# Optimization experiments

Measured on AMD Instinct MI355X. Metric: run time of the kernel, lower is better.

The kernel has to match this reference:

```python
import jax, jax.numpy as jnp
import numpy as np

EPS = 1e-12  # torch F.normalize eps

def setup_inputs() -> dict:
    key = jax.random.key(0)
    k1, k2 = jax.random.split(key)
    N, M, D = 256, 2000, 128
    gene_seq = jax.random.randint(k1, (N, M), 0, 4)
    embedding_mat = jax.random.normal(k2, (M, 4, D), dtype=jnp.float32) * (np.sqrt(2.0) / D)
    return {"gene_seq": gene_seq, "embedding_mat": embedding_mat}

def reference(gene_seq, embedding_mat):
    # L2-normalize each (gene, base) row along embedding dim (torch F.normalize semantics)
    norm = jnp.linalg.norm(embedding_mat, axis=-1, keepdims=True)
    table = embedding_mat / jnp.maximum(norm, EPS)  # (M, 4, D)
    M = table.shape[0]
    # One-hot einsum 'nmi,nmid->nmd' == direct gather of row gene_seq[n,m] at position m
    gene_idx = jnp.arange(M)[None, :]               # (1, M)
    out = table[gene_idx, gene_seq, :]              # (N, M, D)
    return out
```

## Files before the change

### kernel.cpp

```cpp
#include <hip/hip_runtime.h>


#define N_SEQ   256
#define M_GENES 2000
#define D_DIM   128
#define ROWS    (M_GENES * 4)
#define P2_BX   25
#define P2_IT   10

typedef float vfloat4 __attribute__((ext_vector_type(4)));

__global__ __launch_bounds__(256) void inv_norm_kernel(
    const float* __restrict__ emb,
    float*       __restrict__ inv_norm)
{
    const int idx = blockIdx.x * 256 + threadIdx.x;
    const int row = idx >> 5;
    const int c   = idx & 31;

    const vfloat4 v = *reinterpret_cast<const vfloat4*>(emb + ((row << 7) + (c << 2)));
    float ss = v.x * v.x + v.y * v.y + v.z * v.z + v.w * v.w;
    ss += __shfl_xor(ss, 1, 32);
    ss += __shfl_xor(ss, 2, 32);
    ss += __shfl_xor(ss, 4, 32);
    ss += __shfl_xor(ss, 8, 32);
    ss += __shfl_xor(ss, 16, 32);
    const float inv = 1.0f / fmaxf(sqrtf(ss), 1e-12f);
    if (c == 0) inv_norm[row] = inv;
}

__global__ __launch_bounds__(256) void gather_scale_kernel(
    const int*   __restrict__ gene_seq,
    const float* __restrict__ emb,
    const float* __restrict__ inv_norm,
    float*       __restrict__ out)
{
    const int n = blockIdx.y;
    const int* __restrict__ gs = gene_seq + n * M_GENES;
    float* __restrict__ outn = out + (size_t)n * (M_GENES * D_DIM);

    const int j0 = blockIdx.x * 256 + threadIdx.x;

    #pragma unroll
    for (int it = 0; it < P2_IT; ++it) {
        const int j = j0 + it * (P2_BX * 256);
        const int m = j >> 5;
        const int c = j & 31;

        const int   g   = gs[m];
        const int   row = (m << 2) + g;
        const float inv = inv_norm[row];
        const vfloat4 v = *reinterpret_cast<const vfloat4*>(emb + ((row << 7) + (c << 2)));

        vfloat4 o = v * inv;
        __builtin_nontemporal_store(o, reinterpret_cast<vfloat4*>(outn + ((size_t)j << 2)));
    }
}

extern "C" void kernel_launch(void* const* d_in, const int* in_sizes, int n_in,
                              void* d_out, int out_size, void* d_ws, size_t ws_size,
                              hipStream_t stream) {
    const int*   gene_seq = (const int*)d_in[0];
    const float* emb      = (const float*)d_in[1];
    float*       out      = (float*)d_out;
    float*       inv_norm = (float*)d_ws;

    inv_norm_kernel<<<dim3(ROWS * 32 / 256), dim3(256), 0, stream>>>(emb, inv_norm);

    gather_scale_kernel<<<dim3(P2_BX, N_SEQ), dim3(256), 0, stream>>>(
        gene_seq, emb, inv_norm, out);
}
```

Before: 270.8 us.

## Precompute normalized table and XCD-aware tiled gather over gene tiles

The first kernel now writes a fully normalized copy of the embedding table to the workspace, so the gather kernel only copies rows and skips the per-element inv_norm load and multiply. The gather is reorganized into 64-gene tiles per block, with the block id remapped so that each XCD handles a fixed set of four gene tiles across all sequences. Each XCD's L2 then only has to hold a slice of the table. This adds a 4 MB table write, and the last tile needs a bounds-checked path.

```diff
diff --git a/kernel.cpp b/kernel.cpp
--- a/kernel.cpp
+++ b/kernel.cpp
@@ -1,24 +1,26 @@
 #include <hip/hip_runtime.h>
 
 
-#define N_SEQ   256
-#define M_GENES 2000
-#define D_DIM   128
-#define ROWS    (M_GENES * 4)
-#define P2_BX   25
-#define P2_IT   10
+#define N_SEQ     256
+#define M_GENES   2000
+#define D_DIM     128
+#define ROWS      (M_GENES * 4)
+#define P1_BLOCKS (ROWS * 32 / 256)
+#define TILE_M    64
+#define N_TILES   32
+#define P2_IT     8
+#define P2_BLOCKS (N_TILES * N_SEQ)
 
 typedef float vfloat4 __attribute__((ext_vector_type(4)));
 
-__global__ __launch_bounds__(256) void inv_norm_kernel(
+__global__ __launch_bounds__(256) void norm_table_kernel(
     const float* __restrict__ emb,
-    float*       __restrict__ inv_norm)
+    float*       __restrict__ tableN)
 {
     const int idx = blockIdx.x * 256 + threadIdx.x;
-    const int row = idx >> 5;
-    const int c   = idx & 31;
+    const int off = idx << 2;
 
-    const vfloat4 v = *reinterpret_cast<const vfloat4*>(emb + ((row << 7) + (c << 2)));
+    const vfloat4 v = *reinterpret_cast<const vfloat4*>(emb + off);
     float ss = v.x * v.x + v.y * v.y + v.z * v.z + v.w * v.w;
     ss += __shfl_xor(ss, 1, 32);
     ss += __shfl_xor(ss, 2, 32);
@@ -26,34 +28,48 @@
     ss += __shfl_xor(ss, 8, 32);
     ss += __shfl_xor(ss, 16, 32);
     const float inv = 1.0f / fmaxf(sqrtf(ss), 1e-12f);
-    if (c == 0) inv_norm[row] = inv;
+
+    const vfloat4 o = v * inv;
+    *reinterpret_cast<vfloat4*>(tableN + off) = o;
 }
 
-__global__ __launch_bounds__(256) void gather_scale_kernel(
+__global__ __launch_bounds__(256) void gather_kernel(
     const int*   __restrict__ gene_seq,
-    const float* __restrict__ emb,
-    const float* __restrict__ inv_norm,
+    const float* __restrict__ tableN,
     float*       __restrict__ out)
 {
-    const int n = blockIdx.y;
-    const int* __restrict__ gs = gene_seq + n * M_GENES;
-    float* __restrict__ outn = out + (size_t)n * (M_GENES * D_DIM);
+    const int id   = blockIdx.x;
+    const int xcd  = id & 7;
+    const int q    = id >> 3;
+    const int tile = (xcd << 2) | (q >> 8);
+    const int n    = q & 255;
 
-    const int j0 = blockIdx.x * 256 + threadIdx.x;
+    const int* __restrict__ gs   = gene_seq + n * M_GENES;
+    float*     __restrict__ outn = out + (size_t)n * (M_GENES * D_DIM);
+    const int m0 = tile * TILE_M;
 
-    #pragma unroll
-    for (int it = 0; it < P2_IT; ++it) {
-        const int j = j0 + it * (P2_BX * 256);
-        const int m = j >> 5;
-        const int c = j & 31;
-
-        const int   g   = gs[m];
-        const int   row = (m << 2) + g;
-        const float inv = inv_norm[row];
-        const vfloat4 v = *reinterpret_cast<const vfloat4*>(emb + ((row << 7) + (c << 2)));
-
-        vfloat4 o = v * inv;
-        __builtin_nontemporal_store(o, reinterpret_cast<vfloat4*>(outn + ((size_t)j << 2)));
+    if (m0 + TILE_M <= M_GENES) {
+        #pragma unroll
+        for (int it = 0; it < P2_IT; ++it) {
+            const int u   = it * 256 + threadIdx.x;
+            const int m   = m0 + (u >> 5);
+            const int c4  = (u & 31) << 2;
+            const int row = (m << 2) + gs[m];
+            const vfloat4 v = *reinterpret_cast<const vfloat4*>(tableN + (row << 7) + c4);
+            __builtin_nontemporal_store(v, reinterpret_cast<vfloat4*>(outn + (m << 7) + c4));
+        }
+    } else {
+        #pragma unroll
+        for (int it = 0; it < P2_IT; ++it) {
+            const int u = it * 256 + threadIdx.x;
+            const int m = m0 + (u >> 5);
+            if (m < M_GENES) {
+                const int c4  = (u & 31) << 2;
+                const int row = (m << 2) + gs[m];
+                const vfloat4 v = *reinterpret_cast<const vfloat4*>(tableN + (row << 7) + c4);
+                __builtin_nontemporal_store(v, reinterpret_cast<vfloat4*>(outn + (m << 7) + c4));
+            }
+        }
     }
 }
 
@@ -63,10 +79,9 @@
     const int*   gene_seq = (const int*)d_in[0];
     const float* emb      = (const float*)d_in[1];
     float*       out      = (float*)d_out;
-    float*       inv_norm = (float*)d_ws;
+    float*       tableN   = (float*)d_ws;
 
-    inv_norm_kernel<<<dim3(ROWS * 32 / 256), dim3(256), 0, stream>>>(emb, inv_norm);
+    norm_table_kernel<<<dim3(P1_BLOCKS), dim3(256), 0, stream>>>(emb, tableN);
 
-    gather_scale_kernel<<<dim3(P2_BX, N_SEQ), dim3(256), 0, stream>>>(
-        gene_seq, emb, inv_norm, out);
+    gather_kernel<<<dim3(P2_BLOCKS), dim3(256), 0, stream>>>(gene_seq, tableN, out);
 }
```

Measured after the change: 272.0 us. Within noise of the previous version (+0.4%).

## Fuse normalization into gather with per-gene register-resident normalized rows

Applied to the files above, without the earlier changes.

Replaces the two-kernel pipeline (inverse-norm precompute plus gather-and-scale) with one kernel. Each half-wave loads and normalizes all four base rows for one gene into registers, then loops over 64 sequences, picking the row by the gene_seq value broadcast with shuffles. This removes the second launch, the workspace round-trip and the repeated embedding reads per sequence. In exchange, the normalization is recomputed by each of the four sequence-chunk blocks, gene_seq is read with a strided pattern, and output stores change from nontemporal to regular, with each store spread across 64 sequence rows.

```diff
diff --git a/kernel.cpp b/kernel.cpp
--- a/kernel.cpp
+++ b/kernel.cpp
@@ -4,56 +4,58 @@
 #define N_SEQ   256
 #define M_GENES 2000
 #define D_DIM   128
-#define ROWS    (M_GENES * 4)
-#define P2_BX   25
-#define P2_IT   10
+#define GENES_PER_BLOCK 8
+#define N_CHUNK 64
+#define GRID_X  (M_GENES / GENES_PER_BLOCK)
+#define GRID_Y  (N_SEQ / N_CHUNK)
 
 typedef float vfloat4 __attribute__((ext_vector_type(4)));
 
-__global__ __launch_bounds__(256) void inv_norm_kernel(
-    const float* __restrict__ emb,
-    float*       __restrict__ inv_norm)
-{
-    const int idx = blockIdx.x * 256 + threadIdx.x;
-    const int row = idx >> 5;
-    const int c   = idx & 31;
-
-    const vfloat4 v = *reinterpret_cast<const vfloat4*>(emb + ((row << 7) + (c << 2)));
-    float ss = v.x * v.x + v.y * v.y + v.z * v.z + v.w * v.w;
-    ss += __shfl_xor(ss, 1, 32);
-    ss += __shfl_xor(ss, 2, 32);
-    ss += __shfl_xor(ss, 4, 32);
-    ss += __shfl_xor(ss, 8, 32);
-    ss += __shfl_xor(ss, 16, 32);
-    const float inv = 1.0f / fmaxf(sqrtf(ss), 1e-12f);
-    if (c == 0) inv_norm[row] = inv;
-}
-
-__global__ __launch_bounds__(256) void gather_scale_kernel(
+__global__ __launch_bounds__(256) void fused_gather_kernel(
     const int*   __restrict__ gene_seq,
     const float* __restrict__ emb,
-    const float* __restrict__ inv_norm,
     float*       __restrict__ out)
 {
-    const int n = blockIdx.y;
-    const int* __restrict__ gs = gene_seq + n * M_GENES;
-    float* __restrict__ outn = out + (size_t)n * (M_GENES * D_DIM);
+    const int tid  = threadIdx.x;
+    const int wave = tid >> 6;
+    const int lane = tid & 63;
+    const int c    = lane & 31;
 
-    const int j0 = blockIdx.x * 256 + threadIdx.x;
+    const int m0    = blockIdx.x * GENES_PER_BLOCK;
+    const int n0    = blockIdx.y * N_CHUNK;
+    const int m_sel = m0 + (wave << 1) + (lane >> 5);
 
+    vfloat4 r[4];
     #pragma unroll
-    for (int it = 0; it < P2_IT; ++it) {
-        const int j = j0 + it * (P2_BX * 256);
-        const int m = j >> 5;
-        const int c = j & 31;
+    for (int g = 0; g < 4; ++g) {
+        const vfloat4 v = *reinterpret_cast<const vfloat4*>(
+            emb + (((m_sel << 2) + g) << 7) + (c << 2));
+        float ss = v.x * v.x + v.y * v.y + v.z * v.z + v.w * v.w;
+        ss += __shfl_xor(ss, 1, 32);
+        ss += __shfl_xor(ss, 2, 32);
+        ss += __shfl_xor(ss, 4, 32);
+        ss += __shfl_xor(ss, 8, 32);
+        ss += __shfl_xor(ss, 16, 32);
+        const float inv = 1.0f / fmaxf(sqrtf(ss), 1e-12f);
+        r[g] = v * inv;
+    }
 
-        const int   g   = gs[m];
-        const int   row = (m << 2) + g;
-        const float inv = inv_norm[row];
-        const vfloat4 v = *reinterpret_cast<const vfloat4*>(emb + ((row << 7) + (c << 2)));
+    const int g0 = gene_seq[(n0 + c)      * M_GENES + m_sel];
+    const int g1 = gene_seq[(n0 + 32 + c) * M_GENES + m_sel];
 
-        vfloat4 o = v * inv;
-        __builtin_nontemporal_store(o, reinterpret_cast<vfloat4*>(outn + ((size_t)j << 2)));
+    float* __restrict__ outbase = out + (size_t)(m_sel << 7) + (c << 2);
+
+    #pragma unroll 4
+    for (int n = 0; n < N_CHUNK; ++n) {
+        const int src = (lane & 32) | (n & 31);
+        const int gv  = __shfl((n < 32) ? g0 : g1, src, 64);
+
+        const vfloat4 lo = (gv & 1) ? r[1] : r[0];
+        const vfloat4 hi = (gv & 1) ? r[3] : r[2];
+        const vfloat4 v  = (gv & 2) ? hi : lo;
+
+        *reinterpret_cast<vfloat4*>(
+            outbase + (size_t)(n0 + n) * (M_GENES * D_DIM)) = v;
     }
 }
 
@@ -63,10 +65,7 @@
     const int*   gene_seq = (const int*)d_in[0];
     const float* emb      = (const float*)d_in[1];
     float*       out      = (float*)d_out;
-    float*       inv_norm = (float*)d_ws;
 
-    inv_norm_kernel<<<dim3(ROWS * 32 / 256), dim3(256), 0, stream>>>(emb, inv_norm);
-
-    gather_scale_kernel<<<dim3(P2_BX, N_SEQ), dim3(256), 0, stream>>>(
-        gene_seq, emb, inv_norm, out);
+    fused_gather_kernel<<<dim3(GRID_X, GRID_Y), dim3(256), 0, stream>>>(
+        gene_seq, emb, out);
 }
```

Measured after the change: 257.3 us. 5.0% less time.
